# Performance work log

Measured on AMD Instinct MI355X. Metric: run time of the kernel, lower is better.

The kernel has to match this reference:

```python
import jax, jax.numpy as jnp
import numpy as np

DIM = 768
HEADS = 12
HD = DIM // HEADS
SCALE = HD ** -0.5


def setup_inputs() -> dict:
    key = jax.random.key(0)
    ks = jax.random.split(key, 12)
    B, N = 2, 2048
    s = DIM ** -0.5
    return {
        "x1": jax.random.normal(ks[0], (B, N, DIM), jnp.float32),
        "x2": jax.random.normal(ks[1], (B, N, DIM), jnp.float32),
        "Wq": jax.random.normal(ks[2], (DIM, DIM), jnp.float32) * s,
        "bq": jax.random.normal(ks[3], (DIM,), jnp.float32) * 0.01,
        "Wk": jax.random.normal(ks[4], (DIM, DIM), jnp.float32) * s,
        "bk": jax.random.normal(ks[5], (DIM,), jnp.float32) * 0.01,
        "Wv": jax.random.normal(ks[6], (DIM, DIM), jnp.float32) * s,
        "bv": jax.random.normal(ks[7], (DIM,), jnp.float32) * 0.01,
        "Wo": jax.random.normal(ks[8], (DIM, DIM), jnp.float32) * s,
        "bo": jax.random.normal(ks[9], (DIM,), jnp.float32) * 0.01,
        "cross_scale": jnp.array([0.5], jnp.float32),
    }


def _heads(x, W, b):
    # torch Linear: x @ W.T + b; then (B,N,H,hd) -> (B,H,N,hd)
    B, N, _ = x.shape
    y = x @ W.T + b
    return y.reshape(B, N, HEADS, HD).transpose(0, 2, 1, 3)


def reference(x1, x2, Wq, bq, Wk, bk, Wv, bv, Wo, bo, cross_scale):
    B, N, C = x1.shape
    q1, k1, v1 = _heads(x1, Wq, bq), _heads(x1, Wk, bk), _heads(x1, Wv, bv)
    q2, k2, v2 = _heads(x2, Wq, bq), _heads(x2, Wk, bk), _heads(x2, Wv, bv)

    s = cross_scale[0]
    attn11 = jnp.einsum('bhqd,bhkd->bhqk', q1, k1) * SCALE
    attn22 = jnp.einsum('bhqd,bhkd->bhqk', q2, k2) * SCALE
    attn12 = jnp.einsum('bhqd,bhkd->bhqk', q1, k2) * SCALE
    attn21 = jnp.einsum('bhqd,bhkd->bhqk', q2, k1) * SCALE

    a1 = jax.nn.softmax((1.0 - s) * attn11 + s * attn12, axis=-1)
    a2 = jax.nn.softmax((1.0 - s) * attn22 + s * attn21, axis=-1)

    o1 = jnp.einsum('bhqk,bhkd->bhqd', a1, v1).transpose(0, 2, 1, 3).reshape(B, N, C)
    o2 = jnp.einsum('bhqk,bhkd->bhqd', a2, v2).transpose(0, 2, 1, 3).reshape(B, N, C)

    out1 = o1 @ Wo.T + bo
    out2 = o2 @ Wo.T + bo
    return out1, out2
```

## Files before the change

kernel.cpp:

```cpp
#include <hip/hip_runtime.h>

#define KDIM 768
#define HALF 3145728
#define XAELEMS 6291456
#define WELEMS 589824
#define QS 0.18033688f

typedef __attribute__((ext_vector_type(8))) short short8;
typedef __attribute__((ext_vector_type(4))) short short4_;
typedef __attribute__((ext_vector_type(4))) float float4_;
typedef __attribute__((ext_vector_type(2))) unsigned int uint2_;

__device__ __forceinline__ unsigned short f2bf(float f) {
  unsigned int u = __float_as_uint(f);
  u += 0x7fffu + ((u >> 16) & 1u);
  return (unsigned short)(u >> 16);
}

__device__ __forceinline__ unsigned int pack2bf(float a, float b) {
  unsigned int ua = __float_as_uint(a) + 0x8000u;
  unsigned int ub = __float_as_uint(b) + 0x8000u;
  return __builtin_amdgcn_perm(ub, ua, 0x07060302);
}

__device__ __forceinline__ void gll16(const void* g, void* l) {
  __builtin_amdgcn_global_load_lds(
      (const __attribute__((address_space(1))) unsigned int*)g,
      (__attribute__((address_space(3))) unsigned int*)l, 16, 0, 0);
}

#if __has_builtin(__builtin_amdgcn_mfma_f32_16x16x16bf16_1k)
__device__ __forceinline__ float4_ mfma16(short4_ a, short4_ b, float4_ c) {
  return __builtin_amdgcn_mfma_f32_16x16x16bf16_1k(a, b, c, 0, 0, 0);
}
#else
__device__ __forceinline__ float4_ mfma16(short4_ a, short4_ b, float4_ c) {
  asm volatile("v_mfma_f32_16x16x16_bf16 %0, %1, %2, %0\n\ts_nop 7\n\ts_nop 7"
               : "+v"(c) : "v"(a), "v"(b));
  return c;
}
#endif

__global__ void prep_x_kernel(const float* __restrict__ x1, const float* __restrict__ x2,
                              const float* __restrict__ cs,
                              unsigned short* __restrict__ xa, unsigned short* __restrict__ xb) {
  const int i = (blockIdx.x * 256 + threadIdx.x) * 4;
  const float s = cs[0], t_ = 1.0f - s;
  float4 a = *(const float4*)(x1 + i);
  float4 b = *(const float4*)(x2 + i);
  ushort4 ua = { f2bf(a.x), f2bf(a.y), f2bf(a.z), f2bf(a.w) };
  ushort4 ub = { f2bf(b.x), f2bf(b.y), f2bf(b.z), f2bf(b.w) };
  *(ushort4*)(xa + i) = ua;
  *(ushort4*)(xa + HALF + i) = ub;
  ushort4 c1 = { f2bf(t_*a.x + s*b.x), f2bf(t_*a.y + s*b.y), f2bf(t_*a.z + s*b.z), f2bf(t_*a.w + s*b.w) };
  ushort4 c2 = { f2bf(t_*b.x + s*a.x), f2bf(t_*b.y + s*a.y), f2bf(t_*b.z + s*a.z), f2bf(t_*b.w + s*a.w) };
  *(ushort4*)(xb + i) = c1;
  *(ushort4*)(xb + HALF + i) = c2;
}

__global__ void conv_w4_kernel(const float* __restrict__ w0, const float* __restrict__ w1,
                               const float* __restrict__ w2, const float* __restrict__ w3,
                               unsigned short* __restrict__ o0, unsigned short* __restrict__ o1,
                               unsigned short* __restrict__ o2, unsigned short* __restrict__ o3) {
  const int z = blockIdx.y;
  const float* w = (z == 0) ? w0 : (z == 1) ? w1 : (z == 2) ? w2 : w3;
  unsigned short* o = (z == 0) ? o0 : (z == 1) ? o1 : (z == 2) ? o2 : o3;
  const int i = (blockIdx.x * 256 + threadIdx.x) * 4;
  float4 a = *(const float4*)(w + i);
  ushort4 ua = { f2bf(a.x), f2bf(a.y), f2bf(a.z), f2bf(a.w) };
  *(ushort4*)(o + i) = ua;
}

__device__ __forceinline__ void gemm_mainloop(const unsigned short* __restrict__ A,
                                              const unsigned short* __restrict__ W,
                                              unsigned short* As, unsigned short* Bs,
                                              int m0, int n0, int t, float4_ (&acc)[4][4]) {
  const int lane = t & 63, quad = lane >> 4, lrow = lane & 15;
  const int wave = t >> 6;
  const int wm = (wave & 1) * 64, wn = (wave >> 1) * 64;
  for (int kt = 0; kt < KDIM; kt += 64) {
#pragma unroll
    for (int i = 0; i < 4; i++) {
      const int li = i * 256 + t;
      const int row = li >> 3, cc = (li & 7) * 8;
      gll16(A + (size_t)(m0 + row) * KDIM + kt + cc, As + li * 8);
      gll16(W + (size_t)(n0 + row) * KDIM + kt + cc, Bs + li * 8);
    }
    __syncthreads();
#pragma unroll
    for (int kk = 0; kk < 2; kk++) {
      short8 af[4], bfr[4];
#pragma unroll
      for (int i = 0; i < 4; i++)
        af[i] = *(const short8*)(As + (wm + i * 16 + lrow) * 64 + kk * 32 + quad * 8);
#pragma unroll
      for (int j = 0; j < 4; j++)
        bfr[j] = *(const short8*)(Bs + (wn + j * 16 + lrow) * 64 + kk * 32 + quad * 8);
#pragma unroll
      for (int i = 0; i < 4; i++)
#pragma unroll
        for (int j = 0; j < 4; j++)
          acc[i][j] = __builtin_amdgcn_mfma_f32_16x16x32_bf16(af[i], bfr[j], acc[i][j], 0, 0, 0);
    }
    __syncthreads();
  }
}

__global__ __launch_bounds__(256, 2)
void qkv_gemm(const unsigned short* __restrict__ xa, const unsigned short* __restrict__ xb,
              const unsigned short* __restrict__ wq, const unsigned short* __restrict__ wk,
              const unsigned short* __restrict__ wv,
              const float* __restrict__ bq, const float* __restrict__ bk, const float* __restrict__ bv,
              unsigned short* __restrict__ qo, unsigned short* __restrict__ ko,
              unsigned short* __restrict__ vto) {
  __shared__ __align__(16) unsigned short smem[16384];
  unsigned short* As = smem;
  unsigned short* Bs = smem + 8192;
  const int t = threadIdx.x;
  const int z = blockIdx.z;
  const int m0 = blockIdx.x * 128, n0 = blockIdx.y * 128;
  const unsigned short* A = (z == 1) ? xb : xa;
  const unsigned short* W = (z == 0) ? wq : (z == 1) ? wk : wv;
  const float* bias = (z == 0) ? bq : (z == 1) ? bk : bv;
  float4_ acc[4][4];
#pragma unroll
  for (int i = 0; i < 4; i++)
#pragma unroll
    for (int j = 0; j < 4; j++) acc[i][j] = (float4_){0.f, 0.f, 0.f, 0.f};
  gemm_mainloop(A, W, As, Bs, m0, n0, t, acc);

  const int lane = t & 63, quad = lane >> 4, lrow = lane & 15;
  const int wave = t >> 6;
  const int wm = (wave & 1) * 64, wn = (wave >> 1) * 64;

  if (z == 2) {
    unsigned short* Tb = smem + wave * 4096;
#pragma unroll
    for (int i = 0; i < 4; i++) {
#pragma unroll
      for (int j = 0; j < 4; j++) {
        const int nl = j * 16 + lrow;
        const float bn = bias[n0 + wn + nl];
#pragma unroll
        for (int r = 0; r < 4; r++) {
          const int ml = i * 16 + quad * 4 + r;
          const int c = ml >> 3;
          Tb[nl * 64 + ((c ^ (nl & 7)) * 8) + (ml & 7)] = f2bf(acc[i][j][r] + bn);
        }
      }
    }
    __asm__ __volatile__("s_waitcnt lgkmcnt(0)");
    const int sb = (m0 + wm) >> 11;
    const int hh = (n0 + wn) >> 6;
    const int tokbase = ((m0 + wm) & 2047);
#pragma unroll
    for (int i3 = 0; i3 < 8; i3++) {
      const int ci = i3 * 64 + lane;
      const int row = ci >> 3, p = ci & 7;
      short8 rd = *(const short8*)(Tb + row * 64 + p * 8);
      const int c = p ^ (row & 7);
      *(short8*)(vto + ((size_t)(sb * 12 + hh) * 64 + row) * 2048 + tokbase + c * 8) = rd;
    }
  } else {
    unsigned short* dst = (z == 0) ? qo : ko;
    const float scale = (z == 0) ? QS : 1.0f;
#pragma unroll
    for (int i = 0; i < 4; i++) {
#pragma unroll
      for (int j = 0; j < 4; j++) {
        const int n = n0 + wn + j * 16 + lrow;
        const float bn = bias[n];
#pragma unroll
        for (int r = 0; r < 4; r++) {
          const int m = m0 + wm + i * 16 + quad * 4 + r;
          dst[(size_t)m * KDIM + n] = f2bf((acc[i][j][r] + bn) * scale);
        }
      }
    }
  }
}

__global__ __launch_bounds__(256, 2)
void out_gemm(const unsigned short* __restrict__ ob, const unsigned short* __restrict__ wo,
              const float* __restrict__ bo, float* __restrict__ out) {
  __shared__ __align__(16) unsigned short As[128 * 64];
  __shared__ __align__(16) unsigned short Bs[128 * 64];
  const int t = threadIdx.x;
  const int m0 = blockIdx.x * 128, n0 = blockIdx.y * 128;
  float4_ acc[4][4];
#pragma unroll
  for (int i = 0; i < 4; i++)
#pragma unroll
    for (int j = 0; j < 4; j++) acc[i][j] = (float4_){0.f, 0.f, 0.f, 0.f};
  gemm_mainloop(ob, wo, As, Bs, m0, n0, t, acc);

  const int lane = t & 63, quad = lane >> 4, lrow = lane & 15;
  const int wave = t >> 6;
  const int wm = (wave & 1) * 64, wn = (wave >> 1) * 64;
#pragma unroll
  for (int i = 0; i < 4; i++) {
#pragma unroll
    for (int j = 0; j < 4; j++) {
      const int n = n0 + wn + j * 16 + lrow;
      const float bn = bo[n];
#pragma unroll
      for (int r = 0; r < 4; r++) {
        const int m = m0 + wm + i * 16 + quad * 4 + r;
        out[(size_t)m * KDIM + n] = acc[i][j][r] + bn;
      }
    }
  }
}

__global__ __launch_bounds__(256, 2)
void attn_kernel(const unsigned short* __restrict__ qg, const unsigned short* __restrict__ kg,
                 const unsigned short* __restrict__ vt, unsigned short* __restrict__ o) {
  __shared__ __align__(16) unsigned short Ks[2][64 * 64];
  __shared__ __align__(16) unsigned short Vs[2][64 * 64];
  const int prob = blockIdx.x % 48;
  const int q0 = (blockIdx.x / 48) * 128;
  const int sb = prob / 12, h = prob % 12;
  const int t = threadIdx.x, w = t >> 6, lane = t & 63, quad = lane >> 4, lrow = lane & 15;
  const int mbase = sb * 2048;
  const size_t vbase = (size_t)prob * (64 * 2048);

  short8 bq[2][2];
#pragma unroll
  for (int i = 0; i < 2; i++) {
    const unsigned short* qp = qg + (size_t)(mbase + q0 + w * 32 + i * 16 + lrow) * KDIM + h * 64 + quad * 8;
    bq[i][0] = *(const short8*)qp;
    bq[i][1] = *(const short8*)(qp + 32);
  }
  float l_part[2] = {0.f, 0.f};
  float4_ oa[2][4];
#pragma unroll
  for (int i = 0; i < 2; i++)
#pragma unroll
    for (int d = 0; d < 4; d++) oa[i][d] = (float4_){0.f, 0.f, 0.f, 0.f};

  auto stage = [&](int k0, int b) {
#pragma unroll
    for (int i2 = 0; i2 < 2; i2++) {
      const int li = i2 * 256 + t;
      const int row = li >> 3, p = li & 7;
      const int c = p ^ (row & 7);
      gll16(kg + (size_t)(mbase + k0 + row) * KDIM + h * 64 + c * 8, &Ks[b][li * 8]);
    }
#pragma unroll
    for (int i2 = 0; i2 < 2; i2++) {
      const int li = i2 * 256 + t;
      const int row = li >> 3, p = li & 7;
      const int c = p ^ (row & 7);
      gll16(vt + vbase + (size_t)row * 2048 + k0 + c * 8, &Vs[b][li * 8]);
    }
  };
  stage(0, 0);

  for (int kt = 0; kt < 32; kt++) {
    __syncthreads();
    const int b = kt & 1;
    if (kt + 1 < 32) stage((kt + 1) * 64, b ^ 1);

    float4_ st[4][2];
#pragma unroll
    for (int nt = 0; nt < 4; nt++)
#pragma unroll
      for (int i = 0; i < 2; i++) st[nt][i] = (float4_){0.f, 0.f, 0.f, 0.f};
#pragma unroll
    for (int kk = 0; kk < 2; kk++) {
#pragma unroll
      for (int nt = 0; nt < 4; nt++) {
        short8 ak = *(const short8*)(&Ks[b][(nt * 16 + lrow) * 64 + (((kk * 4 + quad) ^ (lrow & 7)) * 8)]);
        st[nt][0] = __builtin_amdgcn_mfma_f32_16x16x32_bf16(ak, bq[0][kk], st[nt][0], 0, 0, 0);
        st[nt][1] = __builtin_amdgcn_mfma_f32_16x16x32_bf16(ak, bq[1][kk], st[nt][1], 0, 0, 0);
      }
    }

    short4_ pb[2][4];
#pragma unroll
    for (int nt = 0; nt < 4; nt++)
#pragma unroll
      for (int i = 0; i < 2; i++) {
        const float p0 = __builtin_amdgcn_exp2f(st[nt][i][0]);
        const float p1 = __builtin_amdgcn_exp2f(st[nt][i][1]);
        const float p2 = __builtin_amdgcn_exp2f(st[nt][i][2]);
        const float p3 = __builtin_amdgcn_exp2f(st[nt][i][3]);
        l_part[i] += (p0 + p1) + (p2 + p3);
        uint2_ uu = { pack2bf(p0, p1), pack2bf(p2, p3) };
        pb[i][nt] = __builtin_bit_cast(short4_, uu);
      }

#pragma unroll
    for (int nt = 0; nt < 4; nt++) {
      const int cp = (((nt * 2 + (quad >> 1)) ^ (lrow & 7)) * 8) + (quad & 1) * 4;
#pragma unroll
      for (int dt = 0; dt < 4; dt++) {
        short4_ av = *(const short4_*)(&Vs[b][(dt * 16 + lrow) * 64 + cp]);
        oa[0][dt] = mfma16(av, pb[0][nt], oa[0][dt]);
        oa[1][dt] = mfma16(av, pb[1][nt], oa[1][dt]);
      }
    }
  }

#pragma unroll
  for (int i = 0; i < 2; i++) {
    float l = l_part[i];
    l += __shfl_xor(l, 16);
    l += __shfl_xor(l, 32);
    const float inv = 1.0f / l;
    const size_t m = (size_t)mbase + q0 + w * 32 + i * 16 + lrow;
#pragma unroll
    for (int dt = 0; dt < 4; dt++) {
      uint2_ uu = { pack2bf(oa[i][dt][0] * inv, oa[i][dt][1] * inv),
                    pack2bf(oa[i][dt][2] * inv, oa[i][dt][3] * inv) };
      *(uint2_*)(o + m * KDIM + h * 64 + dt * 16 + quad * 4) = uu;
    }
  }
}

extern "C" void kernel_launch(void* const* d_in, const int* in_sizes, int n_in,
                              void* d_out, int out_size, void* d_ws, size_t ws_size,
                              hipStream_t stream) {
  const float* x1 = (const float*)d_in[0];
  const float* x2 = (const float*)d_in[1];
  const float* Wq = (const float*)d_in[2];
  const float* bq = (const float*)d_in[3];
  const float* Wk = (const float*)d_in[4];
  const float* bk = (const float*)d_in[5];
  const float* Wv = (const float*)d_in[6];
  const float* bv = (const float*)d_in[7];
  const float* Wo = (const float*)d_in[8];
  const float* bo = (const float*)d_in[9];
  const float* cs = (const float*)d_in[10];
  float* out = (float*)d_out;

  char* ws = (char*)d_ws;
  size_t off = 0;
  auto alloc = [&](size_t bytes) {
    void* p = ws + off;
    off += (bytes + 255) & ~(size_t)255;
    return p;
  };
  unsigned short* xa  = (unsigned short*)alloc((size_t)XAELEMS * 2);
  unsigned short* xb  = (unsigned short*)alloc((size_t)XAELEMS * 2);
  unsigned short* wqb = (unsigned short*)alloc((size_t)WELEMS * 2);
  unsigned short* wkb = (unsigned short*)alloc((size_t)WELEMS * 2);
  unsigned short* wvb = (unsigned short*)alloc((size_t)WELEMS * 2);
  unsigned short* wob = (unsigned short*)alloc((size_t)WELEMS * 2);
  unsigned short* qg  = (unsigned short*)alloc((size_t)XAELEMS * 2);
  unsigned short* kgb = (unsigned short*)alloc((size_t)XAELEMS * 2);
  unsigned short* vtb = (unsigned short*)alloc((size_t)XAELEMS * 2);
  unsigned short* ob  = (unsigned short*)alloc((size_t)XAELEMS * 2);

  prep_x_kernel<<<HALF / 1024, 256, 0, stream>>>(x1, x2, cs, xa, xb);
  conv_w4_kernel<<<dim3(WELEMS / 1024, 4), 256, 0, stream>>>(Wq, Wk, Wv, Wo, wqb, wkb, wvb, wob);
  qkv_gemm<<<dim3(64, 6, 3), 256, 0, stream>>>(xa, xb, wqb, wkb, wvb, bq, bk, bv, qg, kgb, vtb);
  attn_kernel<<<48 * 16, 256, 0, stream>>>(qg, kgb, vtb, ob);
  out_gemm<<<dim3(64, 6), 256, 0, stream>>>(ob, wob, bo, out);
}
```

Baseline: 226.6 us.

## Widen GEMM K-tile with swizzled LDS, stage Q/K stores, fuse attention row sums

The GEMM mainloop now loads 128-wide K tiles into XOR-swizzled shared memory, which halves the barrier count and is meant to cut LDS bank conflicts, at the cost of doubling LDS per block. The Q/K epilogue of the projection GEMM goes through a per-wave LDS transpose so it can write coalesced 16-byte stores instead of scalar bf16 stores. The attention kernel interleaves QK^T, exp and PV per 16-key subtile to lower register pressure, raises the launch bound to 3 blocks per SM, and computes the softmax denominator with an MFMA against a ones vector instead of VALU adds and shuffles. That denominator now sums the bf16-rounded probabilities, a small numerical change.

```diff
diff --git a/kernel.cpp b/kernel.cpp
--- a/kernel.cpp
+++ b/kernel.cpp
@@ -78,24 +78,26 @@
   const int lane = t & 63, quad = lane >> 4, lrow = lane & 15;
   const int wave = t >> 6;
   const int wm = (wave & 1) * 64, wn = (wave >> 1) * 64;
-  for (int kt = 0; kt < KDIM; kt += 64) {
-#pragma unroll
-    for (int i = 0; i < 4; i++) {
+  for (int kt = 0; kt < KDIM; kt += 128) {
+#pragma unroll
+    for (int i = 0; i < 8; i++) {
       const int li = i * 256 + t;
-      const int row = li >> 3, cc = (li & 7) * 8;
-      gll16(A + (size_t)(m0 + row) * KDIM + kt + cc, As + li * 8);
-      gll16(W + (size_t)(n0 + row) * KDIM + kt + cc, Bs + li * 8);
+      const int row = li >> 4, p = li & 15;
+      const int c = p ^ (row & 7);
+      gll16(A + (size_t)(m0 + row) * KDIM + kt + c * 8, As + li * 8);
+      gll16(W + (size_t)(n0 + row) * KDIM + kt + c * 8, Bs + li * 8);
     }
     __syncthreads();
 #pragma unroll
-    for (int kk = 0; kk < 2; kk++) {
+    for (int kk = 0; kk < 4; kk++) {
+      const int phys = ((kk * 4 + quad) ^ (lrow & 7)) * 8;
       short8 af[4], bfr[4];
 #pragma unroll
       for (int i = 0; i < 4; i++)
-        af[i] = *(const short8*)(As + (wm + i * 16 + lrow) * 64 + kk * 32 + quad * 8);
+        af[i] = *(const short8*)(As + (wm + i * 16 + lrow) * 128 + phys);
 #pragma unroll
       for (int j = 0; j < 4; j++)
-        bfr[j] = *(const short8*)(Bs + (wn + j * 16 + lrow) * 64 + kk * 32 + quad * 8);
+        bfr[j] = *(const short8*)(Bs + (wn + j * 16 + lrow) * 128 + phys);
 #pragma unroll
       for (int i = 0; i < 4; i++)
 #pragma unroll
@@ -113,9 +115,9 @@
               const float* __restrict__ bq, const float* __restrict__ bk, const float* __restrict__ bv,
               unsigned short* __restrict__ qo, unsigned short* __restrict__ ko,
               unsigned short* __restrict__ vto) {
-  __shared__ __align__(16) unsigned short smem[16384];
+  __shared__ __align__(16) unsigned short smem[32768];
   unsigned short* As = smem;
-  unsigned short* Bs = smem + 8192;
+  unsigned short* Bs = smem + 16384;
   const int t = threadIdx.x;
   const int z = blockIdx.z;
   const int m0 = blockIdx.x * 128, n0 = blockIdx.y * 128;
@@ -164,18 +166,29 @@
   } else {
     unsigned short* dst = (z == 0) ? qo : ko;
     const float scale = (z == 0) ? QS : 1.0f;
+    unsigned short* Tb = smem + wave * 4096;
 #pragma unroll
     for (int i = 0; i < 4; i++) {
 #pragma unroll
       for (int j = 0; j < 4; j++) {
-        const int n = n0 + wn + j * 16 + lrow;
-        const float bn = bias[n];
+        const int nl = j * 16 + lrow;
+        const float bn = bias[n0 + wn + nl];
+        const int clog = nl >> 3, lo = nl & 7;
 #pragma unroll
         for (int r = 0; r < 4; r++) {
-          const int m = m0 + wm + i * 16 + quad * 4 + r;
-          dst[(size_t)m * KDIM + n] = f2bf((acc[i][j][r] + bn) * scale);
+          const int ml = i * 16 + quad * 4 + r;
+          Tb[ml * 64 + ((clog ^ (ml & 7)) * 8) + lo] = f2bf((acc[i][j][r] + bn) * scale);
         }
       }
+    }
+    __asm__ __volatile__("s_waitcnt lgkmcnt(0)");
+#pragma unroll
+    for (int i3 = 0; i3 < 8; i3++) {
+      const int ci = i3 * 64 + lane;
+      const int ml = ci >> 3, p = ci & 7;
+      short8 rd = *(const short8*)(Tb + ml * 64 + p * 8);
+      const int clog = p ^ (ml & 7);
+      *(short8*)(dst + (size_t)(m0 + wm + ml) * KDIM + n0 + wn + clog * 8) = rd;
     }
   }
 }
@@ -183,8 +196,8 @@
 __global__ __launch_bounds__(256, 2)
 void out_gemm(const unsigned short* __restrict__ ob, const unsigned short* __restrict__ wo,
               const float* __restrict__ bo, float* __restrict__ out) {
-  __shared__ __align__(16) unsigned short As[128 * 64];
-  __shared__ __align__(16) unsigned short Bs[128 * 64];
+  __shared__ __align__(16) unsigned short As[128 * 128];
+  __shared__ __align__(16) unsigned short Bs[128 * 128];
   const int t = threadIdx.x;
   const int m0 = blockIdx.x * 128, n0 = blockIdx.y * 128;
   float4_ acc[4][4];
@@ -212,7 +225,7 @@
   }
 }
 
-__global__ __launch_bounds__(256, 2)
+__global__ __launch_bounds__(256, 3)
 void attn_kernel(const unsigned short* __restrict__ qg, const unsigned short* __restrict__ kg,
                  const unsigned short* __restrict__ vt, unsigned short* __restrict__ o) {
   __shared__ __align__(16) unsigned short Ks[2][64 * 64];
@@ -231,7 +244,8 @@
     bq[i][0] = *(const short8*)qp;
     bq[i][1] = *(const short8*)(qp + 32);
   }
-  float l_part[2] = {0.f, 0.f};
+  const short4_ ones = { (short)0x3F80, (short)0x3F80, (short)0x3F80, (short)0x3F80 };
+  float4_ lacc[2] = { (float4_){0.f,0.f,0.f,0.f}, (float4_){0.f,0.f,0.f,0.f} };
   float4_ oa[2][4];
 #pragma unroll
   for (int i = 0; i < 2; i++)
@@ -261,53 +275,39 @@
     const int b = kt & 1;
     if (kt + 1 < 32) stage((kt + 1) * 64, b ^ 1);
 
-    float4_ st[4][2];
-#pragma unroll
-    for (int nt = 0; nt < 4; nt++)
-#pragma unroll
-      for (int i = 0; i < 2; i++) st[nt][i] = (float4_){0.f, 0.f, 0.f, 0.f};
-#pragma unroll
-    for (int kk = 0; kk < 2; kk++) {
-#pragma unroll
-      for (int nt = 0; nt < 4; nt++) {
-        short8 ak = *(const short8*)(&Ks[b][(nt * 16 + lrow) * 64 + (((kk * 4 + quad) ^ (lrow & 7)) * 8)]);
-        st[nt][0] = __builtin_amdgcn_mfma_f32_16x16x32_bf16(ak, bq[0][kk], st[nt][0], 0, 0, 0);
-        st[nt][1] = __builtin_amdgcn_mfma_f32_16x16x32_bf16(ak, bq[1][kk], st[nt][1], 0, 0, 0);
-      }
-    }
-
-    short4_ pb[2][4];
-#pragma unroll
-    for (int nt = 0; nt < 4; nt++)
-#pragma unroll
-      for (int i = 0; i < 2; i++) {
-        const float p0 = __builtin_amdgcn_exp2f(st[nt][i][0]);
-        const float p1 = __builtin_amdgcn_exp2f(st[nt][i][1]);
-        const float p2 = __builtin_amdgcn_exp2f(st[nt][i][2]);
-        const float p3 = __builtin_amdgcn_exp2f(st[nt][i][3]);
-        l_part[i] += (p0 + p1) + (p2 + p3);
-        uint2_ uu = { pack2bf(p0, p1), pack2bf(p2, p3) };
-        pb[i][nt] = __builtin_bit_cast(short4_, uu);
-      }
-
 #pragma unroll
     for (int nt = 0; nt < 4; nt++) {
+      const unsigned short* krow = &Ks[b][(nt * 16 + lrow) * 64];
+      short8 ak0 = *(const short8*)(krow + ((quad ^ (lrow & 7)) * 8));
+      short8 ak1 = *(const short8*)(krow + (((4 + quad) ^ (lrow & 7)) * 8));
+      float4_ st0 = __builtin_amdgcn_mfma_f32_16x16x32_bf16(ak0, bq[0][0], (float4_){0.f,0.f,0.f,0.f}, 0, 0, 0);
+      float4_ st1 = __builtin_amdgcn_mfma_f32_16x16x32_bf16(ak0, bq[1][0], (float4_){0.f,0.f,0.f,0.f}, 0, 0, 0);
+      st0 = __builtin_amdgcn_mfma_f32_16x16x32_bf16(ak1, bq[0][1], st0, 0, 0, 0);
+      st1 = __builtin_amdgcn_mfma_f32_16x16x32_bf16(ak1, bq[1][1], st1, 0, 0, 0);
+
+      uint2_ u0 = { pack2bf(__builtin_amdgcn_exp2f(st0[0]), __builtin_amdgcn_exp2f(st0[1])),
+                    pack2bf(__builtin_amdgcn_exp2f(st0[2]), __builtin_amdgcn_exp2f(st0[3])) };
+      uint2_ u1 = { pack2bf(__builtin_amdgcn_exp2f(st1[0]), __builtin_amdgcn_exp2f(st1[1])),
+                    pack2bf(__builtin_amdgcn_exp2f(st1[2]), __builtin_amdgcn_exp2f(st1[3])) };
+      short4_ pb0 = __builtin_bit_cast(short4_, u0);
+      short4_ pb1 = __builtin_bit_cast(short4_, u1);
+
+      lacc[0] = mfma16(ones, pb0, lacc[0]);
+      lacc[1] = mfma16(ones, pb1, lacc[1]);
+
       const int cp = (((nt * 2 + (quad >> 1)) ^ (lrow & 7)) * 8) + (quad & 1) * 4;
 #pragma unroll
       for (int dt = 0; dt < 4; dt++) {
         short4_ av = *(const short4_*)(&Vs[b][(dt * 16 + lrow) * 64 + cp]);
-        oa[0][dt] = mfma16(av, pb[0][nt], oa[0][dt]);
-        oa[1][dt] = mfma16(av, pb[1][nt], oa[1][dt]);
+        oa[0][dt] = mfma16(av, pb0, oa[0][dt]);
+        oa[1][dt] = mfma16(av, pb1, oa[1][dt]);
       }
     }
   }
 
 #pragma unroll
   for (int i = 0; i < 2; i++) {
-    float l = l_part[i];
-    l += __shfl_xor(l, 16);
-    l += __shfl_xor(l, 32);
-    const float inv = 1.0f / l;
+    const float inv = 1.0f / lacc[i][0];
     const size_t m = (size_t)mbase + q0 + w * 32 + i * 16 + lrow;
 #pragma unroll
     for (int dt = 0; dt < 4; dt++) {
```

Measured after the change: 229.1 us. About the same (+1.1%).

## Merge prep kernels, load GEMM weights directly from global, stage Q/K stores via LDS

Applied to the files above, without the earlier changes.

Fuses the activation and weight bf16 conversion kernels into one launch. The GEMM main loop now stages only the A tile in LDS with an XOR swizzle and a 128-wide K step, and reads the weight fragments straight from global memory. Occupancy hints rise to 3 blocks per SM. The Q/K epilogue writes through an LDS transpose buffer so global stores become 16-byte coalesced. The direct global weight loads may add latency that the kernel no longer hides through LDS, in exchange for less LDS traffic and fewer syncs.

```diff
diff --git a/kernel.cpp b/kernel.cpp
--- a/kernel.cpp
+++ b/kernel.cpp
@@ -41,61 +41,65 @@
 }
 #endif
 
-__global__ void prep_x_kernel(const float* __restrict__ x1, const float* __restrict__ x2,
-                              const float* __restrict__ cs,
-                              unsigned short* __restrict__ xa, unsigned short* __restrict__ xb) {
-  const int i = (blockIdx.x * 256 + threadIdx.x) * 4;
-  const float s = cs[0], t_ = 1.0f - s;
-  float4 a = *(const float4*)(x1 + i);
-  float4 b = *(const float4*)(x2 + i);
-  ushort4 ua = { f2bf(a.x), f2bf(a.y), f2bf(a.z), f2bf(a.w) };
-  ushort4 ub = { f2bf(b.x), f2bf(b.y), f2bf(b.z), f2bf(b.w) };
-  *(ushort4*)(xa + i) = ua;
-  *(ushort4*)(xa + HALF + i) = ub;
-  ushort4 c1 = { f2bf(t_*a.x + s*b.x), f2bf(t_*a.y + s*b.y), f2bf(t_*a.z + s*b.z), f2bf(t_*a.w + s*b.w) };
-  ushort4 c2 = { f2bf(t_*b.x + s*a.x), f2bf(t_*b.y + s*a.y), f2bf(t_*b.z + s*a.z), f2bf(t_*b.w + s*a.w) };
-  *(ushort4*)(xb + i) = c1;
-  *(ushort4*)(xb + HALF + i) = c2;
-}
-
-__global__ void conv_w4_kernel(const float* __restrict__ w0, const float* __restrict__ w1,
-                               const float* __restrict__ w2, const float* __restrict__ w3,
-                               unsigned short* __restrict__ o0, unsigned short* __restrict__ o1,
-                               unsigned short* __restrict__ o2, unsigned short* __restrict__ o3) {
-  const int z = blockIdx.y;
-  const float* w = (z == 0) ? w0 : (z == 1) ? w1 : (z == 2) ? w2 : w3;
-  unsigned short* o = (z == 0) ? o0 : (z == 1) ? o1 : (z == 2) ? o2 : o3;
-  const int i = (blockIdx.x * 256 + threadIdx.x) * 4;
-  float4 a = *(const float4*)(w + i);
-  ushort4 ua = { f2bf(a.x), f2bf(a.y), f2bf(a.z), f2bf(a.w) };
-  *(ushort4*)(o + i) = ua;
-}
-
-__device__ __forceinline__ void gemm_mainloop(const unsigned short* __restrict__ A,
-                                              const unsigned short* __restrict__ W,
-                                              unsigned short* As, unsigned short* Bs,
-                                              int m0, int n0, int t, float4_ (&acc)[4][4]) {
+__global__ void init_kernel(const float* __restrict__ x1, const float* __restrict__ x2,
+                            const float* __restrict__ cs,
+                            const float* __restrict__ w0, const float* __restrict__ w1,
+                            const float* __restrict__ w2, const float* __restrict__ w3,
+                            unsigned short* __restrict__ xa, unsigned short* __restrict__ xb,
+                            unsigned short* __restrict__ o0, unsigned short* __restrict__ o1,
+                            unsigned short* __restrict__ o2, unsigned short* __restrict__ o3) {
+  const int bid = blockIdx.x;
+  if (bid < 3072) {
+    const int i = (bid * 256 + threadIdx.x) * 4;
+    const float s = cs[0], t_ = 1.0f - s;
+    float4 a = *(const float4*)(x1 + i);
+    float4 b = *(const float4*)(x2 + i);
+    ushort4 ua = { f2bf(a.x), f2bf(a.y), f2bf(a.z), f2bf(a.w) };
+    ushort4 ub = { f2bf(b.x), f2bf(b.y), f2bf(b.z), f2bf(b.w) };
+    *(ushort4*)(xa + i) = ua;
+    *(ushort4*)(xa + HALF + i) = ub;
+    ushort4 c1 = { f2bf(t_*a.x + s*b.x), f2bf(t_*a.y + s*b.y), f2bf(t_*a.z + s*b.z), f2bf(t_*a.w + s*b.w) };
+    ushort4 c2 = { f2bf(t_*b.x + s*a.x), f2bf(t_*b.y + s*a.y), f2bf(t_*b.z + s*a.z), f2bf(t_*b.w + s*a.w) };
+    *(ushort4*)(xb + i) = c1;
+    *(ushort4*)(xb + HALF + i) = c2;
+  } else {
+    const int zz = (bid - 3072) / 576;
+    const float* w = (zz == 0) ? w0 : (zz == 1) ? w1 : (zz == 2) ? w2 : w3;
+    unsigned short* o = (zz == 0) ? o0 : (zz == 1) ? o1 : (zz == 2) ? o2 : o3;
+    const int i = (((bid - 3072) % 576) * 256 + threadIdx.x) * 4;
+    float4 a = *(const float4*)(w + i);
+    ushort4 ua = { f2bf(a.x), f2bf(a.y), f2bf(a.z), f2bf(a.w) };
+    *(ushort4*)(o + i) = ua;
+  }
+}
+
+__device__ __forceinline__ void gemm_mainloop2(const unsigned short* __restrict__ A,
+                                               const unsigned short* __restrict__ W,
+                                               unsigned short* As,
+                                               int m0, int n0, int t, float4_ (&acc)[4][4]) {
   const int lane = t & 63, quad = lane >> 4, lrow = lane & 15;
   const int wave = t >> 6;
   const int wm = (wave & 1) * 64, wn = (wave >> 1) * 64;
-  for (int kt = 0; kt < KDIM; kt += 64) {
-#pragma unroll
-    for (int i = 0; i < 4; i++) {
+  const unsigned short* wbase = W + (size_t)(n0 + wn + lrow) * KDIM + quad * 8;
+  for (int kt = 0; kt < KDIM; kt += 128) {
+#pragma unroll
+    for (int i = 0; i < 8; i++) {
       const int li = i * 256 + t;
-      const int row = li >> 3, cc = (li & 7) * 8;
-      gll16(A + (size_t)(m0 + row) * KDIM + kt + cc, As + li * 8);
-      gll16(W + (size_t)(n0 + row) * KDIM + kt + cc, Bs + li * 8);
+      const int row = li >> 4, p = li & 15;
+      const int c = p ^ (row & 7);
+      gll16(A + (size_t)(m0 + row) * KDIM + kt + c * 8, As + li * 8);
     }
     __syncthreads();
 #pragma unroll
-    for (int kk = 0; kk < 2; kk++) {
+    for (int kk = 0; kk < 4; kk++) {
+      const int phys = ((kk * 4 + quad) ^ (lrow & 7)) * 8;
       short8 af[4], bfr[4];
 #pragma unroll
+      for (int j = 0; j < 4; j++)
+        bfr[j] = *(const short8*)(wbase + (size_t)(j * 16) * KDIM + kt + kk * 32);
+#pragma unroll
       for (int i = 0; i < 4; i++)
-        af[i] = *(const short8*)(As + (wm + i * 16 + lrow) * 64 + kk * 32 + quad * 8);
-#pragma unroll
-      for (int j = 0; j < 4; j++)
-        bfr[j] = *(const short8*)(Bs + (wn + j * 16 + lrow) * 64 + kk * 32 + quad * 8);
+        af[i] = *(const short8*)(As + (wm + i * 16 + lrow) * 128 + phys);
 #pragma unroll
       for (int i = 0; i < 4; i++)
 #pragma unroll
@@ -106,7 +110,7 @@
   }
 }
 
-__global__ __launch_bounds__(256, 2)
+__global__ __launch_bounds__(256, 3)
 void qkv_gemm(const unsigned short* __restrict__ xa, const unsigned short* __restrict__ xb,
               const unsigned short* __restrict__ wq, const unsigned short* __restrict__ wk,
               const unsigned short* __restrict__ wv,
@@ -114,8 +118,6 @@
               unsigned short* __restrict__ qo, unsigned short* __restrict__ ko,
               unsigned short* __restrict__ vto) {
   __shared__ __align__(16) unsigned short smem[16384];
-  unsigned short* As = smem;
-  unsigned short* Bs = smem + 8192;
   const int t = threadIdx.x;
   const int z = blockIdx.z;
   const int m0 = blockIdx.x * 128, n0 = blockIdx.y * 128;
@@ -127,7 +129,7 @@
   for (int i = 0; i < 4; i++)
 #pragma unroll
     for (int j = 0; j < 4; j++) acc[i][j] = (float4_){0.f, 0.f, 0.f, 0.f};
-  gemm_mainloop(A, W, As, Bs, m0, n0, t, acc);
+  gemm_mainloop2(A, W, smem, m0, n0, t, acc);
 
   const int lane = t & 63, quad = lane >> 4, lrow = lane & 15;
   const int wave = t >> 6;
@@ -164,27 +166,37 @@
   } else {
     unsigned short* dst = (z == 0) ? qo : ko;
     const float scale = (z == 0) ? QS : 1.0f;
+    unsigned short* Tb = smem + wave * 4096;
 #pragma unroll
     for (int i = 0; i < 4; i++) {
 #pragma unroll
       for (int j = 0; j < 4; j++) {
-        const int n = n0 + wn + j * 16 + lrow;
-        const float bn = bias[n];
+        const int nl = j * 16 + lrow;
+        const float bn = bias[n0 + wn + nl];
+        const int clog = nl >> 3, lo = nl & 7;
 #pragma unroll
         for (int r = 0; r < 4; r++) {
-          const int m = m0 + wm + i * 16 + quad * 4 + r;
-          dst[(size_t)m * KDIM + n] = f2bf((acc[i][j][r] + bn) * scale);
+          const int ml = i * 16 + quad * 4 + r;
+          Tb[ml * 64 + ((clog ^ (ml & 7)) * 8) + lo] = f2bf((acc[i][j][r] + bn) * scale);
         }
       }
     }
-  }
-}
-
-__global__ __launch_bounds__(256, 2)
+    __asm__ __volatile__("s_waitcnt lgkmcnt(0)");
+#pragma unroll
+    for (int i3 = 0; i3 < 8; i3++) {
+      const int ci = i3 * 64 + lane;
+      const int ml = ci >> 3, p = ci & 7;
+      short8 rd = *(const short8*)(Tb + ml * 64 + p * 8);
+      const int clog = p ^ (ml & 7);
+      *(short8*)(dst + (size_t)(m0 + wm + ml) * KDIM + n0 + wn + clog * 8) = rd;
+    }
+  }
+}
+
+__global__ __launch_bounds__(256, 3)
 void out_gemm(const unsigned short* __restrict__ ob, const unsigned short* __restrict__ wo,
               const float* __restrict__ bo, float* __restrict__ out) {
-  __shared__ __align__(16) unsigned short As[128 * 64];
-  __shared__ __align__(16) unsigned short Bs[128 * 64];
+  __shared__ __align__(16) unsigned short As[128 * 128];
   const int t = threadIdx.x;
   const int m0 = blockIdx.x * 128, n0 = blockIdx.y * 128;
   float4_ acc[4][4];
@@ -192,7 +204,7 @@
   for (int i = 0; i < 4; i++)
 #pragma unroll
     for (int j = 0; j < 4; j++) acc[i][j] = (float4_){0.f, 0.f, 0.f, 0.f};
-  gemm_mainloop(ob, wo, As, Bs, m0, n0, t, acc);
+  gemm_mainloop2(ob, wo, As, m0, n0, t, acc);
 
   const int lane = t & 63, quad = lane >> 4, lrow = lane & 15;
   const int wave = t >> 6;
@@ -352,8 +364,7 @@
   unsigned short* vtb = (unsigned short*)alloc((size_t)XAELEMS * 2);
   unsigned short* ob  = (unsigned short*)alloc((size_t)XAELEMS * 2);
 
-  prep_x_kernel<<<HALF / 1024, 256, 0, stream>>>(x1, x2, cs, xa, xb);
-  conv_w4_kernel<<<dim3(WELEMS / 1024, 4), 256, 0, stream>>>(Wq, Wk, Wv, Wo, wqb, wkb, wvb, wob);
+  init_kernel<<<5376, 256, 0, stream>>>(x1, x2, cs, Wq, Wk, Wv, Wo, xa, xb, wqb, wkb, wvb, wob);
   qkv_gemm<<<dim3(64, 6, 3), 256, 0, stream>>>(xa, xb, wqb, wkb, wvb, bq, bk, bv, qg, kgb, vtb);
   attn_kernel<<<48 * 16, 256, 0, stream>>>(qg, kgb, vtb, ob);
   out_gemm<<<dim3(64, 6), 256, 0, stream>>>(ob, wob, bo, out);
```

After: 254.7 us. +12.4%, slower.
